# Kernel tuning notes

Measured on AMD Instinct MI355X. Metric: run time of the kernel, lower is better.

Reference implementation:

```python
import jax, jax.numpy as jnp
import numpy as np

EPS = 1e-5
ABIT = 8
WBIT = 8


def ste_round(x):
    # straight-through rounding (HAWQ SymmetricQuantFunction)
    return x + jax.lax.stop_gradient(jnp.round(x) - x)


def quant_act(x, bit=ABIT):
    # per-tensor symmetric activation quantization (QuantAct)
    n = 2.0 ** (bit - 1) - 1  # 127
    scale = jnp.max(jnp.abs(x)) / n
    x_int = jnp.clip(ste_round(x / scale), -n - 1, n)
    return x_int * scale, scale


def setup_inputs() -> dict:
    key = jax.random.key(0)
    k = jax.random.split(key, 6)
    B, C_in, H, W, C_out = 32, 512, 32, 32, 128
    x = jax.random.normal(k[0], (B, C_in, H, W), jnp.float32)
    # incoming activation scale (input assumed already 8-bit quantized)
    act_scaling_factor = (jnp.max(jnp.abs(x)) / 127.0).reshape(1)
    bn_gamma = jax.random.uniform(k[1], (C_in,), jnp.float32, 0.5, 1.5)
    bn_beta = jax.random.normal(k[2], (C_in,), jnp.float32) * 0.1
    bn_mean = jax.random.normal(k[3], (C_in,), jnp.float32) * 0.1
    bn_var = jax.random.uniform(k[4], (C_in,), jnp.float32, 0.5, 1.5)
    conv_weight = jax.random.normal(k[5], (C_out, C_in, 3, 3), jnp.float32) / np.sqrt(C_in * 9)
    return {"x": x, "act_scaling_factor": act_scaling_factor,
            "bn_gamma": bn_gamma, "bn_beta": bn_beta,
            "bn_mean": bn_mean, "bn_var": bn_var,
            "conv_weight": conv_weight}


def reference(x, act_scaling_factor, bn_gamma, bn_beta, bn_mean, bn_var, conv_weight):
    nw = 2.0 ** (WBIT - 1) - 1  # 127
    s_in = act_scaling_factor.reshape(())

    # ---- QuantBn: fold BN into per-channel affine, quantize weight/bias ----
    w_bn = bn_gamma / jnp.sqrt(bn_var + EPS)            # [C_in]
    b_bn = bn_beta - bn_mean * w_bn                      # [C_in]
    ws_bn = jnp.max(jnp.abs(w_bn)) / nw                  # per-tensor weight scale
    w_int = jnp.clip(ste_round(w_bn / ws_bn), -nw - 1, nw)
    bn_sf = ws_bn * s_in                                 # bn output scaling factor
    b_int = ste_round(b_bn / bn_sf)
    x_int = x / s_in
    x = (x_int * w_int[None, :, None, None] + b_int[None, :, None, None]) * bn_sf

    # ---- ReLU ----
    x = jax.nn.relu(x)

    # ---- QuantAct: requantize activations to 8 bit ----
    x, s_act = quant_act(x)

    # ---- QuantConv2d: per-output-channel 8-bit weight quant, int conv ----
    ws_c = jnp.max(jnp.abs(conv_weight), axis=(1, 2, 3)) / nw       # [C_out]
    w_cint = jnp.clip(ste_round(conv_weight / ws_c[:, None, None, None]), -nw - 1, nw)
    y_int = jax.lax.conv_general_dilated(
        x / s_act, w_cint, window_strides=(1, 1), padding=((1, 1), (1, 1)),
        dimension_numbers=("NCHW", "OIHW", "NCHW"))
    conv_sf = s_act * ws_c                               # [C_out]
    y = y_int * conv_sf[None, :, None, None]

    # ---- QuantAct output requant ----
    y, s_out = quant_act(y)
    return (y, s_out)
```

## Files before the change

kernel.cpp:

```cpp
#include <hip/hip_runtime.h>


typedef int v4i __attribute__((ext_vector_type(4)));

#define WS_A1    64
#define WS_B1    2112
#define WS_WSC   4160
#define WS_XMX   4672
#define WS_XMN   6720
#define WS_WQ    8768
#define WS_X2    598592
#define WS_ZROW  18424384

__device__ __forceinline__ float wave_max(float m) {
#pragma unroll
    for (int off = 32; off; off >>= 1) m = fmaxf(m, __shfl_xor(m, off));
    return m;
}

__device__ __forceinline__ void stage16(const char* g, char* s, int lane) {
#if defined(__has_builtin) && __has_builtin(__builtin_amdgcn_global_load_lds)
    __builtin_amdgcn_global_load_lds(
        (const __attribute__((address_space(1))) void*)g,
        (__attribute__((address_space(3))) void*)s, 16, 0, 0);
#else
    *(v4i*)(s + lane * 16) = *(const v4i*)g;
#endif
}

__global__ __launch_bounds__(512) void k_prep(
    const float* __restrict__ gamma, const float* __restrict__ beta,
    const float* __restrict__ mean,  const float* __restrict__ var,
    const float* __restrict__ asf,   const float* __restrict__ cw,
    const float4* __restrict__ x4,
    float* ws_f, unsigned* ws_u, float* __restrict__ wsc,
    signed char* __restrict__ wq) {
    int t = threadIdx.x;
    int bid = blockIdx.x;
    __shared__ float red[16];
    if (bid < 512) {
        int c = bid;
        float mx = -3.4e38f, mn = 3.4e38f;
#pragma unroll
        for (int r = 0; r < 16; ++r) {
            int bbb = r * 2 + (t >> 8);
            float4 v = x4[((size_t)(bbb * 512 + c)) * 256 + (t & 255)];
            mx = fmaxf(mx, fmaxf(fmaxf(v.x, v.y), fmaxf(v.z, v.w)));
            mn = fminf(mn, fminf(fminf(v.x, v.y), fminf(v.z, v.w)));
        }
        mx = wave_max(mx);
        mn = -wave_max(-mn);
        if ((t & 63) == 0) { red[t >> 6] = mx; red[8 + (t >> 6)] = mn; }
        __syncthreads();
        if (t == 0) {
            float M = red[0], N = red[8];
#pragma unroll
            for (int i = 1; i < 8; ++i) { M = fmaxf(M, red[i]); N = fminf(N, red[8 + i]); }
            ws_f[WS_XMX / 4 + c] = M;
            ws_f[WS_XMN / 4 + c] = N;
        }
    } else if (bid < 640) {
        int co = bid - 512;
        const float* w = cw + (size_t)co * 4608;
        float m = 0.f;
        for (int j = t; j < 4608; j += 512) m = fmaxf(m, fabsf(w[j]));
        m = wave_max(m);
        if ((t & 63) == 0) red[t >> 6] = m;
        __syncthreads();
        float mall = red[0];
#pragma unroll
        for (int i = 1; i < 8; ++i) mall = fmaxf(mall, red[i]);
        float sc = mall / 127.0f;
        if (t == 0) wsc[co] = sc;
        int ci = t >> 6, cq = (t >> 4) & 3, cb = t & 15;
#pragma unroll
        for (int tap = 0; tap < 9; ++tap) {
            float q = fminf(fmaxf(rintf(w[t * 9 + tap] / sc), -128.f), 127.f);
            wq[(((size_t)(tap * 8 + ci) * 4 + cq) * 128 + co) * 16 + cb] = (signed char)q;
        }
    } else {
        float wbn = gamma[t] / sqrtf(var[t] + 1e-5f);
        float bbn = beta[t] - mean[t] * wbn;
        float m = wave_max(fabsf(wbn));
        if ((t & 63) == 0) red[t >> 6] = m;
        __syncthreads();
        float mall = red[0];
#pragma unroll
        for (int i = 1; i < 8; ++i) mall = fmaxf(mall, red[i]);
        float ws_bn = mall / 127.0f;
        float s_in  = asf[0];
        float bn_sf = ws_bn * s_in;
        float wint  = fminf(fmaxf(rintf(wbn / ws_bn), -128.f), 127.f);
        float bint  = rintf(bbn / bn_sf);
        ws_f[WS_A1 / 4 + t] = wint * bn_sf / s_in;
        ws_f[WS_B1 / 4 + t] = bint * bn_sf;
        if (t == 0) ws_u[1] = 0u;
    }
}

__global__ __launch_bounds__(256) void k_xquant(
    const float4* __restrict__ x4, float* __restrict__ ws_f,
    unsigned* __restrict__ x2u, unsigned* __restrict__ zrowu) {
    int bb = 31 - (blockIdx.x >> 5), h = blockIdx.x & 31;
    const float* A1 = ws_f + WS_A1 / 4;
    const float* B1 = ws_f + WS_B1 / 4;
    const float* XMX = ws_f + WS_XMX / 4;
    const float* XMN = ws_f + WS_XMN / 4;
    int t = threadIdx.x;

    __shared__ float sred[4];
    float cand = 0.f;
#pragma unroll
    for (int c0 = 0; c0 < 512; c0 += 256) {
        int c = c0 + t;
        float A = A1[c], B = B1[c];
        cand = fmaxf(cand, fmaxf(fmaf(XMX[c], A, B), fmaf(XMN[c], A, B)));
    }
    cand = wave_max(cand);
    if ((t & 63) == 0) sred[t >> 6] = cand;
    __syncthreads();
    float xm = fmaxf(fmaxf(sred[0], sred[1]), fmaxf(sred[2], sred[3]));
    float inv_sact = 127.0f / xm;
    if (blockIdx.x == 0 && t == 0) ws_f[3] = xm / 127.0f;

    size_t rowd = (size_t)(bb * 32 + h) * 4352;
    {
        int p = t >> 3, side = (t >> 2) & 1, d = t & 3;
        x2u[rowd + (p * 34 + side * 33) * 4 + d] = 0u;
    }
    if (blockIdx.x < 17) {
        int idx = blockIdx.x * 256 + t;
        if (idx < 4352) zrowu[idx] = 0u;
    }

    __shared__ unsigned lds[512 * 9];

#pragma unroll
    for (int it = 0; it < 16; ++it) {
        int idx = it * 256 + t;
        int c = idx >> 3, f4 = idx & 7;
        float4 v = x4[((size_t)bb * 512 + c) * 256 + h * 8 + f4];
        float A = A1[c] * inv_sact, B = B1[c] * inv_sact;
        unsigned q0 = (unsigned)(int)fminf(rintf(fmaxf(fmaf(v.x, A, B), 0.f)), 127.f);
        unsigned q1 = (unsigned)(int)fminf(rintf(fmaxf(fmaf(v.y, A, B), 0.f)), 127.f);
        unsigned q2 = (unsigned)(int)fminf(rintf(fmaxf(fmaf(v.z, A, B), 0.f)), 127.f);
        unsigned q3 = (unsigned)(int)fminf(rintf(fmaxf(fmaf(v.w, A, B), 0.f)), 127.f);
        lds[c * 9 + f4] = q0 | (q1 << 8) | (q2 << 16) | (q3 << 24);
    }
    __syncthreads();

#pragma unroll
    for (int it = 0; it < 4; ++it) {
        int p = it * 8 + (t >> 5);
        int s = (t >> 2) & 7;
        int k = t & 3;
        unsigned L[16];
#pragma unroll
        for (int j = 0; j < 16; ++j) L[j] = lds[(p * 16 + j) * 9 + s];
        uint4 o;
        unsigned* op = (unsigned*)&o;
#pragma unroll
        for (int d = 0; d < 4; ++d)
            op[d] = ((L[4 * d] >> (8 * k)) & 255u) |
                    (((L[4 * d + 1] >> (8 * k)) & 255u) << 8) |
                    (((L[4 * d + 2] >> (8 * k)) & 255u) << 16) |
                    (((L[4 * d + 3] >> (8 * k)) & 255u) << 24);
        *(uint4*)(x2u + rowd + (size_t)(p * 34 + s * 4 + 1 + k) * 4) = o;
    }
}

__global__ __launch_bounds__(256, 2) void k_conv(
    const unsigned char* __restrict__ x2, const unsigned char* __restrict__ zrow,
    const signed char* __restrict__ wq,
    const float* __restrict__ wsc, const float* __restrict__ ws_f,
    unsigned* __restrict__ amaxy, float* __restrict__ y) {
    __shared__ char ldsb[73728];
    int t = threadIdx.x;
    int lane = t & 63, wv = t >> 6;
    int wh = wv & 1, rp = wv >> 1;
    int m = lane & 15, quad = lane >> 4;

    int bid = blockIdx.x;
    int tile = (bid & 7) * 64 + (bid >> 3);
    int ch = tile & 1;
    int rg = (tile >> 1) & 7;
    int bb = tile >> 4;
    int co0 = ch * 64;
    int h0 = rg * 4 + rp * 2;

    const unsigned char* xb = x2 + (size_t)bb * (32 * 17408);
    const v4i* rpt[4];
#pragma unroll
    for (int j = 0; j < 4; ++j) {
        int row = h0 - 1 + j;
        rpt[j] = (const v4i*)(((unsigned)row < 32u) ? (xb + (size_t)row * 17408) : zrow);
    }

    v4i acc[2][4];
#pragma unroll
    for (int i = 0; i < 2; ++i)
#pragma unroll
        for (int j = 0; j < 4; ++j) acc[i][j] = (v4i){0, 0, 0, 0};

    int abase = quad * 34 + m + wh * 16;

#pragma unroll
    for (int i = 0; i < 9; ++i) {
        int c = wv * 9 + i;
        int tap = c >> 2, cq = c & 3;
        const char* g = (const char*)wq +
            ((((size_t)(tap * 8 + 0) * 4 + cq) * 128 + co0) * 16) + lane * 16;
        stage16(g, ldsb + (c << 10), lane);
    }
    __syncthreads();

#pragma unroll
    for (int ci = 0; ci < 8; ++ci) {
        if (ci < 7) {
#pragma unroll
            for (int i = 0; i < 9; ++i) {
                int c = wv * 9 + i;
                int tap = c >> 2, cq = c & 3;
                const char* g = (const char*)wq +
                    ((((size_t)(tap * 8 + ci + 1) * 4 + cq) * 128 + co0) * 16) + lane * 16;
                stage16(g, ldsb + ((ci + 1) & 1) * 36864 + (c << 10), lane);
            }
        }
        const v4i* bv = (const v4i*)(ldsb + (ci & 1) * 36864);
#pragma unroll
        for (int kh = 0; kh < 3; ++kh)
#pragma unroll
            for (int kw = 0; kw < 3; ++kw) {
                int tap = kh * 3 + kw;
                v4i a0 = rpt[kh][ci * 136 + abase + kw];
                v4i a1 = rpt[kh + 1][ci * 136 + abase + kw];
#pragma unroll
                for (int nt = 0; nt < 4; ++nt) {
                    v4i bf = bv[(tap * 4 + quad) * 64 + nt * 16 + m];
                    acc[0][nt] = __builtin_amdgcn_mfma_i32_16x16x64_i8(a0, bf, acc[0][nt], 0, 0, 0);
                    acc[1][nt] = __builtin_amdgcn_mfma_i32_16x16x64_i8(a1, bf, acc[1][nt], 0, 0, 0);
                }
            }
        __syncthreads();
    }

    float s_act = ws_f[3];
    float mx = 0.f;
#pragma unroll
    for (int nt = 0; nt < 4; ++nt) {
        int co = co0 + nt * 16 + m;
        float sf = s_act * wsc[co];
#pragma unroll
        for (int r = 0; r < 2; ++r) {
            int row = h0 + r;
            float* yb = y + ((size_t)(bb * 128 + co)) * 1024 + row * 32 + wh * 16;
            float4 vv;
            vv.x = (float)acc[r][nt][0] * sf;
            vv.y = (float)acc[r][nt][1] * sf;
            vv.z = (float)acc[r][nt][2] * sf;
            vv.w = (float)acc[r][nt][3] * sf;
            *(float4*)(yb + quad * 4) = vv;
            mx = fmaxf(mx, fmaxf(fmaxf(fabsf(vv.x), fabsf(vv.y)),
                                 fmaxf(fabsf(vv.z), fabsf(vv.w))));
        }
    }
    mx = wave_max(mx);
    if (lane == 0) ((float*)ldsb)[wv] = mx;
    __syncthreads();
    if (t == 0) {
        float* r = (float*)ldsb;
        float M = fmaxf(fmaxf(r[0], r[1]), fmaxf(r[2], r[3]));
        atomicMax(amaxy, __float_as_uint(M));
    }
}

__global__ __launch_bounds__(256) void k_yquant(float* __restrict__ yout,
                                                const unsigned* __restrict__ ws_u) {
    float s_out = __uint_as_float(ws_u[1]) / 127.0f;
    float4* y4 = (float4*)yout;
    int stride = gridDim.x * blockDim.x;
    for (int i = blockIdx.x * blockDim.x + threadIdx.x; i < 1048576; i += stride) {
        float4 v = y4[i];
        v.x = fminf(fmaxf(rintf(v.x / s_out), -128.f), 127.f) * s_out;
        v.y = fminf(fmaxf(rintf(v.y / s_out), -128.f), 127.f) * s_out;
        v.z = fminf(fmaxf(rintf(v.z / s_out), -128.f), 127.f) * s_out;
        v.w = fminf(fmaxf(rintf(v.w / s_out), -128.f), 127.f) * s_out;
        y4[i] = v;
    }
    if (blockIdx.x == 0 && threadIdx.x == 0) yout[4194304] = s_out;
}

extern "C" void kernel_launch(void* const* d_in, const int* in_sizes, int n_in,
                              void* d_out, int out_size, void* d_ws, size_t ws_size,
                              hipStream_t stream) {
    const float* x     = (const float*)d_in[0];
    const float* asf   = (const float*)d_in[1];
    const float* gamma = (const float*)d_in[2];
    const float* beta  = (const float*)d_in[3];
    const float* mean  = (const float*)d_in[4];
    const float* var   = (const float*)d_in[5];
    const float* cw    = (const float*)d_in[6];

    float*    ws_f = (float*)d_ws;
    unsigned* ws_u = (unsigned*)d_ws;
    signed char*   wq   = (signed char*)d_ws + WS_WQ;
    unsigned char* x2   = (unsigned char*)d_ws + WS_X2;
    unsigned char* zrow = (unsigned char*)d_ws + WS_ZROW;
    float* y = (float*)d_out;

    k_prep<<<641, 512, 0, stream>>>(gamma, beta, mean, var, asf, cw,
                                    (const float4*)x, ws_f, ws_u,
                                    ws_f + WS_WSC / 4, wq);
    k_xquant<<<1024, 256, 0, stream>>>((const float4*)x, ws_f,
                                       (unsigned*)x2, (unsigned*)zrow);
    k_conv<<<512, 256, 0, stream>>>(x2, zrow, wq, ws_f + WS_WSC / 4,
                                    ws_f, ws_u + 1, y);
    k_yquant<<<1024, 256, 0, stream>>>(y, ws_u);
}
```

Before: 159.2 us.

## Enlarge conv tile to 8 rows per block with register-reused A across kh taps

Measured after the change: 154.2 us. 3.1% less time.

```diff
diff --git a/kernel.cpp b/kernel.cpp
--- a/kernel.cpp
+++ b/kernel.cpp
@@ -169,7 +169,7 @@
     }
 }
 
-__global__ __launch_bounds__(256, 2) void k_conv(
+__global__ __launch_bounds__(512, 2) void k_conv(
     const unsigned char* __restrict__ x2, const unsigned char* __restrict__ zrow,
     const signed char* __restrict__ wq,
     const float* __restrict__ wsc, const float* __restrict__ ws_f,
@@ -177,81 +177,107 @@
     __shared__ char ldsb[73728];
     int t = threadIdx.x;
     int lane = t & 63, wv = t >> 6;
-    int wh = wv & 1, rp = wv >> 1;
+    int nh = wv & 1;
+    int wh = (wv >> 1) & 1;
+    int rq = wv >> 2;
     int m = lane & 15, quad = lane >> 4;
 
     int bid = blockIdx.x;
-    int tile = (bid & 7) * 64 + (bid >> 3);
+    int tile = (bid & 7) * 32 + (bid >> 3);
     int ch = tile & 1;
-    int rg = (tile >> 1) & 7;
-    int bb = tile >> 4;
+    int rg = (tile >> 1) & 3;
+    int bb = tile >> 3;
     int co0 = ch * 64;
-    int h0 = rg * 4 + rp * 2;
+    int h0 = rg * 8 + rq * 4;
 
     const unsigned char* xb = x2 + (size_t)bb * (32 * 17408);
-    const v4i* rpt[4];
-#pragma unroll
-    for (int j = 0; j < 4; ++j) {
+    const v4i* rpt[6];
+#pragma unroll
+    for (int j = 0; j < 6; ++j) {
         int row = h0 - 1 + j;
         rpt[j] = (const v4i*)(((unsigned)row < 32u) ? (xb + (size_t)row * 17408) : zrow);
     }
 
-    v4i acc[2][4];
-#pragma unroll
-    for (int i = 0; i < 2; ++i)
-#pragma unroll
-        for (int j = 0; j < 4; ++j) acc[i][j] = (v4i){0, 0, 0, 0};
+    v4i acc[4][2];
+#pragma unroll
+    for (int i = 0; i < 4; ++i)
+#pragma unroll
+        for (int j = 0; j < 2; ++j) acc[i][j] = (v4i){0, 0, 0, 0};
 
     int abase = quad * 34 + m + wh * 16;
 
-#pragma unroll
-    for (int i = 0; i < 9; ++i) {
-        int c = wv * 9 + i;
-        int tap = c >> 2, cq = c & 3;
-        const char* g = (const char*)wq +
-            ((((size_t)(tap * 8 + 0) * 4 + cq) * 128 + co0) * 16) + lane * 16;
-        stage16(g, ldsb + (c << 10), lane);
-    }
-    __syncthreads();
-
-#pragma unroll
-    for (int ci = 0; ci < 8; ++ci) {
-        if (ci < 7) {
-#pragma unroll
-            for (int i = 0; i < 9; ++i) {
-                int c = wv * 9 + i;
+    auto stage_ci = [&](int cig, int buf) {
+#pragma unroll
+        for (int i = 0; i < 5; ++i) {
+            int c = i * 8 + wv;
+            if (c < 36) {
                 int tap = c >> 2, cq = c & 3;
                 const char* g = (const char*)wq +
-                    ((((size_t)(tap * 8 + ci + 1) * 4 + cq) * 128 + co0) * 16) + lane * 16;
-                stage16(g, ldsb + ((ci + 1) & 1) * 36864 + (c << 10), lane);
+                    ((((size_t)(tap * 8 + cig) * 4 + cq) * 128 + co0) * 16) + lane * 16;
+                stage16(g, ldsb + buf * 36864 + (c << 10), lane);
             }
         }
+    };
+
+    stage_ci(0, 0);
+    __syncthreads();
+
+#pragma unroll
+    for (int ci = 0; ci < 8; ++ci) {
         const v4i* bv = (const v4i*)(ldsb + (ci & 1) * 36864);
-#pragma unroll
-        for (int kh = 0; kh < 3; ++kh)
+
+        v4i A[6][3];
+#pragma unroll
+        for (int j = 0; j < 6; ++j)
+#pragma unroll
+            for (int kw = 0; kw < 3; ++kw)
+                A[j][kw] = rpt[j][ci * 136 + abase + kw];
+
+        auto load_Bk = [&](v4i(&B)[3][2], int kh) {
+#pragma unroll
+            for (int kw = 0; kw < 3; ++kw)
+#pragma unroll
+                for (int nt = 0; nt < 2; ++nt)
+                    B[kw][nt] = bv[((kh * 3 + kw) * 4 + quad) * 64 + nh * 32 + nt * 16 + m];
+        };
+        auto mfma_kh = [&](const v4i(&Ar0)[3], const v4i(&Ar1)[3],
+                           const v4i(&Ar2)[3], const v4i(&Ar3)[3],
+                           const v4i(&B)[3][2]) {
+            __builtin_amdgcn_s_setprio(1);
 #pragma unroll
             for (int kw = 0; kw < 3; ++kw) {
-                int tap = kh * 3 + kw;
-                v4i a0 = rpt[kh][ci * 136 + abase + kw];
-                v4i a1 = rpt[kh + 1][ci * 136 + abase + kw];
-#pragma unroll
-                for (int nt = 0; nt < 4; ++nt) {
-                    v4i bf = bv[(tap * 4 + quad) * 64 + nt * 16 + m];
-                    acc[0][nt] = __builtin_amdgcn_mfma_i32_16x16x64_i8(a0, bf, acc[0][nt], 0, 0, 0);
-                    acc[1][nt] = __builtin_amdgcn_mfma_i32_16x16x64_i8(a1, bf, acc[1][nt], 0, 0, 0);
-                }
+                acc[0][0] = __builtin_amdgcn_mfma_i32_16x16x64_i8(Ar0[kw], B[kw][0], acc[0][0], 0, 0, 0);
+                acc[0][1] = __builtin_amdgcn_mfma_i32_16x16x64_i8(Ar0[kw], B[kw][1], acc[0][1], 0, 0, 0);
+                acc[1][0] = __builtin_amdgcn_mfma_i32_16x16x64_i8(Ar1[kw], B[kw][0], acc[1][0], 0, 0, 0);
+                acc[1][1] = __builtin_amdgcn_mfma_i32_16x16x64_i8(Ar1[kw], B[kw][1], acc[1][1], 0, 0, 0);
+                acc[2][0] = __builtin_amdgcn_mfma_i32_16x16x64_i8(Ar2[kw], B[kw][0], acc[2][0], 0, 0, 0);
+                acc[2][1] = __builtin_amdgcn_mfma_i32_16x16x64_i8(Ar2[kw], B[kw][1], acc[2][1], 0, 0, 0);
+                acc[3][0] = __builtin_amdgcn_mfma_i32_16x16x64_i8(Ar3[kw], B[kw][0], acc[3][0], 0, 0, 0);
+                acc[3][1] = __builtin_amdgcn_mfma_i32_16x16x64_i8(Ar3[kw], B[kw][1], acc[3][1], 0, 0, 0);
             }
+            __builtin_amdgcn_s_setprio(0);
+        };
+
+        v4i B0[3][2], B1[3][2], B2[3][2];
+        load_Bk(B0, 0);
+        load_Bk(B1, 1);
+        if (ci < 7) stage_ci(ci + 1, (ci + 1) & 1);
+        mfma_kh(A[0], A[1], A[2], A[3], B0);
+        load_Bk(B2, 2);
+        mfma_kh(A[1], A[2], A[3], A[4], B1);
+        mfma_kh(A[2], A[3], A[4], A[5], B2);
+
         __syncthreads();
     }
 
     float s_act = ws_f[3];
     float mx = 0.f;
 #pragma unroll
-    for (int nt = 0; nt < 4; ++nt) {
-        int co = co0 + nt * 16 + m;
+    for (int nt = 0; nt < 2; ++nt) {
+        int co = co0 + nh * 32 + nt * 16 + m;
         float sf = s_act * wsc[co];
 #pragma unroll
-        for (int r = 0; r < 2; ++r) {
+        for (int r = 0; r < 4; ++r) {
             int row = h0 + r;
             float* yb = y + ((size_t)(bb * 128 + co)) * 1024 + row * 32 + wh * 16;
             float4 vv;
@@ -269,7 +295,9 @@
     __syncthreads();
     if (t == 0) {
         float* r = (float*)ldsb;
-        float M = fmaxf(fmaxf(r[0], r[1]), fmaxf(r[2], r[3]));
+        float M = r[0];
+#pragma unroll
+        for (int i = 1; i < 8; ++i) M = fmaxf(M, r[i]);
         atomicMax(amaxy, __float_as_uint(M));
     }
 }
@@ -313,7 +341,7 @@
                                     ws_f + WS_WSC / 4, wq);
     k_xquant<<<1024, 256, 0, stream>>>((const float4*)x, ws_f,
                                        (unsigned*)x2, (unsigned*)zrow);
-    k_conv<<<512, 256, 0, stream>>>(x2, zrow, wq, ws_f + WS_WSC / 4,
+    k_conv<<<256, 512, 0, stream>>>(x2, zrow, wq, ws_f + WS_WSC / 4,
                                     ws_f, ws_u + 1, y);
     k_yquant<<<1024, 256, 0, stream>>>(y, ws_u);
 }
```
